# Optimization experiments

Measured on AMD Instinct MI355X. Metric: run time of the kernel, lower is better.

Reference implementation:

```python
import jax, jax.numpy as jnp
import numpy as np
from jax import lax

STEPS = 16
CHANNELS = 64
HIDDEN = 1024
LENGTH = 2048
BATCH = 32
EPS = 1e-5

def setup_inputs() -> dict:
    key = jax.random.key(0)
    ks = jax.random.split(key, 8)
    x = jax.random.normal(ks[0], (BATCH, CHANNELS, LENGTH), dtype=jnp.float32)
    # Conv1d params (PyTorch layout OIH for weights)
    s1 = 1.0 / np.sqrt(CHANNELS * 3)
    s2 = 1.0 / np.sqrt(HIDDEN)
    w1 = jax.random.uniform(ks[1], (HIDDEN, CHANNELS, 3), jnp.float32, -s1, s1)
    b1 = jax.random.uniform(ks[2], (HIDDEN,), jnp.float32, -s1, s1)
    w2 = jax.random.uniform(ks[3], (HIDDEN, HIDDEN), jnp.float32, -s2, s2)
    b2 = jax.random.uniform(ks[4], (HIDDEN,), jnp.float32, -s2, s2)
    w3 = jax.random.uniform(ks[5], (CHANNELS, HIDDEN), jnp.float32, -s2, s2)
    b3 = jax.random.uniform(ks[6], (CHANNELS,), jnp.float32, -s2, s2)
    # LayerNorm([channels, length]) elementwise affine
    gamma = jnp.ones((CHANNELS, LENGTH), dtype=jnp.float32)
    beta = jnp.zeros((CHANNELS, LENGTH), dtype=jnp.float32)
    return {"x": x, "w1": w1, "b1": b1, "w2": w2, "b2": b2,
            "w3": w3, "b3": b3, "gamma": gamma, "beta": beta}

def reference(x, w1, b1, w2, b2, w3, b3, gamma, beta):
    # Eval-mode forward: dropout is identity, no noise injection.
    def step(x, _):
        # conv1: k=3, pad=1  -> [B, HIDDEN, L]
        h = lax.conv_general_dilated(
            x, w1, window_strides=(1,), padding=[(1, 1)],
            dimension_numbers=("NCH", "OIH", "NCH"))
        h = jax.nn.relu(h + b1[None, :, None])
        # conv2: 1x1 (pointwise) -> GEMM over channel dim
        h = jnp.einsum("oh,bhl->bol", w2, h) + b2[None, :, None]
        h = jax.nn.relu(h)
        # conv3: 1x1 back to channels
        h = jnp.einsum("ch,bhl->bcl", w3, h) + b3[None, :, None]
        x = x + h  # residual
        # LayerNorm over [channels, length] per sample
        mu = jnp.mean(x, axis=(1, 2), keepdims=True)
        var = jnp.var(x, axis=(1, 2), keepdims=True)
        x = (x - mu) * lax.rsqrt(var + EPS) * gamma[None] + beta[None]
        return x, None

    x, _ = lax.scan(step, x, None, length=STEPS)
    return x
```

## Files before the change

### kernel.cpp

```cpp
#include <hip/hip_runtime.h>
#include <stdint.h>

#define L_LEN 2048
#define LP (L_LEN + 2)
#define CH 64
#define HID 1024
#define NSTEP 16
#define NB 32
#define EPS_F 1e-5f

typedef __bf16 bf16x8 __attribute__((ext_vector_type(8)));
typedef float f32x4 __attribute__((ext_vector_type(4)));

__device__ __forceinline__ float u16f(unsigned short u){
  unsigned int x = ((unsigned int)u) << 16;
  return __builtin_bit_cast(float, x);
}
__device__ __forceinline__ unsigned short f2u(float f){
  unsigned int x = __builtin_bit_cast(unsigned int, f);
  unsigned int r = x + 0x7FFFu + ((x >> 16) & 1u);
  return (unsigned short)(r >> 16);
}

__device__ __forceinline__ void gload16(const unsigned short* g, const unsigned short* l){
  __builtin_amdgcn_global_load_lds(
      (const __attribute__((address_space(1))) unsigned int*)g,
      (__attribute__((address_space(3))) unsigned int*)l, 16, 0, 0);
}

__global__ void flag_k(const unsigned int* __restrict__ gamma, int* __restrict__ flag){
  *flag = (gamma[0] == 0x3F803F80u) ? 1 : 0;
}

__global__ __launch_bounds__(256)
void conv_k(const void* __restrict__ src, unsigned short* __restrict__ dst, int n,
            const int* __restrict__ flagp){
  int fl = *flagp;
  for (int i = blockIdx.x * 256 + threadIdx.x; i < n; i += gridDim.x * 256){
    dst[i] = fl ? ((const unsigned short*)src)[i] : f2u(((const float*)src)[i]);
  }
}

__global__ __launch_bounds__(256)
void packw1_k(const void* __restrict__ w1, unsigned short* __restrict__ w1p,
              const int* __restrict__ flagp){
  int idx = blockIdx.x * 256 + threadIdx.x;
  int o = idx / 192;
  int r = idx - o * 192;
  int t = r >> 6;
  int c = r & 63;
  int sidx = (o * 64 + c) * 3 + t;
  w1p[idx] = (*flagp) ? ((const unsigned short*)w1)[sidx]
                      : f2u(((const float*)w1)[sidx]);
}

__global__ __launch_bounds__(256)
void pad_k(unsigned short* __restrict__ xbfT){
  int i = blockIdx.x * 256 + threadIdx.x;
  int s = i >> 7;
  int r = i & 127;
  size_t row = (r >> 6) ? (size_t)(LP - 1) : 0;
  xbfT[((size_t)s * LP + row) * CH + (r & 63)] = 0;
}

__global__ __launch_bounds__(256)
void init_k(const void* __restrict__ xin, float* __restrict__ xf,
            unsigned short* __restrict__ xbfT, const int* __restrict__ flagp){
  int t = blockIdx.x * 256 + threadIdx.x;
  size_t i0 = (size_t)t * 4;
  float4 f;
  if (*flagp){
    ushort4 v = *reinterpret_cast<const ushort4*>(&((const unsigned short*)xin)[i0]);
    f = make_float4(u16f(v.x), u16f(v.y), u16f(v.z), u16f(v.w));
  } else {
    f = *reinterpret_cast<const float4*>(&((const float*)xin)[i0]);
  }
  *reinterpret_cast<float4*>(&xf[i0]) = f;
  int s = (int)(i0 >> 17);
  int r = (int)(i0 & 131071);
  int c = r >> 11;
  int l = r & 2047;
  unsigned short* d = &xbfT[((size_t)s * LP + l + 1) * CH + c];
  d[0]      = f2u(f.x);
  d[CH]     = f2u(f.y);
  d[2 * CH] = f2u(f.z);
  d[3 * CH] = f2u(f.w);
}


template<int QM>
__device__ __forceinline__ void ld_a(const unsigned short* lb, int wm, int lane,
                                     bf16x8 (&af)[4][2]){
  #pragma unroll
  for (int i = 0; i < 4; i++)
    #pragma unroll
    for (int kk = 0; kk < 2; kk++){
      int r  = wm * 128 + QM * 64 + i * 16 + (lane & 15);
      int cb = kk * 4 + (lane >> 4);
      af[i][kk] = *reinterpret_cast<const bf16x8*>(lb + r * 64 + ((cb ^ (r & 7)) << 3));
    }
}
template<int QN>
__device__ __forceinline__ void ld_b(const unsigned short* lb, int wn, int lane,
                                     bf16x8 (&bfr)[2][2][2]){
  #pragma unroll
  for (int j = 0; j < 2; j++)
    #pragma unroll
    for (int kk = 0; kk < 2; kk++){
      int r  = wn * 64 + QN * 32 + j * 16 + (lane & 15);
      int cb = kk * 4 + (lane >> 4);
      bfr[QN][j][kk] = *reinterpret_cast<const bf16x8*>(lb + 16384 + r * 64 + ((cb ^ (r & 7)) << 3));
    }
}
template<int QM, int QN>
__device__ __forceinline__ void mfma_q(f32x4 (&acc)[8][4], bf16x8 (&af)[4][2],
                                       bf16x8 (&bfr)[2][2][2]){
  #pragma unroll
  for (int i = 0; i < 4; i++)
    #pragma unroll
    for (int j = 0; j < 2; j++)
      #pragma unroll
      for (int kk = 0; kk < 2; kk++)
        acc[QM * 4 + i][QN * 2 + j] = __builtin_amdgcn_mfma_f32_16x16x32_bf16(
            af[i][kk], bfr[QN][j][kk], acc[QM * 4 + i][QN * 2 + j], 0, 0, 0);
}

#define SYNC_MID() do { __builtin_amdgcn_s_barrier(); \
  asm volatile("s_waitcnt lgkmcnt(0)" ::: "memory"); \
  __builtin_amdgcn_sched_barrier(0); \
  __builtin_amdgcn_s_setprio(1); } while(0)
#define SYNC_END0() do { __builtin_amdgcn_s_setprio(0); \
  __builtin_amdgcn_s_barrier(); } while(0)
#define SYNC_ENDV() do { __builtin_amdgcn_s_setprio(0); \
  asm volatile("s_waitcnt vmcnt(4)" ::: "memory"); \
  __builtin_amdgcn_s_barrier(); } while(0)

__global__ __launch_bounds__(512, 2)
void gemm8_k(const unsigned short* __restrict__ A,
             const unsigned short* __restrict__ Bx,
             const unsigned short* __restrict__ bias,
             unsigned short* __restrict__ OutB)
{
  __shared__ __align__(16) unsigned short lds[65536];
  const int tid  = threadIdx.x;
  const int lane = tid & 63;
  const int wave = tid >> 6;
  const int wm   = wave >> 2;
  const int wn   = wave & 3;

  const int nwg = gridDim.x;
  const int bid = blockIdx.x;
  const int qq = nwg >> 3, rr = nwg & 7;
  const int xcd = bid & 7, loc = bid >> 3;
  const int wg = (xcd < rr) ? (xcd * (qq + 1) + loc)
                            : (rr * (qq + 1) + (xcd - rr) * qq + loc);
  const int bx = wg & 3;
  const int t_ = wg >> 2;
  const int by = t_ & 7;
  const int bb = t_ >> 3;
  const int m0 = bx * 256;
  const int n0 = by * 256;

  const unsigned short* Bb = Bx + (size_t)bb * L_LEN * HID;

  f32x4 acc[8][4];
  #pragma unroll
  for (int i = 0; i < 8; i++)
    #pragma unroll
    for (int j = 0; j < 4; j++)
      #pragma unroll
      for (int v = 0; v < 4; v++) acc[i][j][v] = 0.f;

  bf16x8 af[4][2];
  bf16x8 bfr[2][2][2];

  auto STAGE_A = [&](int t, int buf, int half){
    #pragma unroll
    for (int li = 0; li < 2; li++){
      int q = li * 512 + tid;
      int row = q >> 3, cc = q & 7;
      int scc = cc ^ (row & 7);
      gload16(&A[(size_t)(m0 + half * 128 + row) * HID + t * 64 + scc * 8],
              lds + buf * 32768 + half * 8192 + (li * 512 + wave * 64) * 8);
    }
  };
  auto STAGE_B = [&](int t, int buf, int half){
    #pragma unroll
    for (int li = 0; li < 2; li++){
      int q = li * 512 + tid;
      int row = q >> 3, cc = q & 7;
      int scc = cc ^ (row & 7);
      gload16(&Bb[(size_t)(n0 + half * 128 + row) * HID + t * 64 + scc * 8],
              lds + buf * 32768 + 16384 + half * 8192 + (li * 512 + wave * 64) * 8);
    }
  };

  const unsigned short* L0 = lds;
  const unsigned short* L1 = lds + 32768;

  STAGE_B(0, 0, 0); STAGE_B(0, 0, 1);
  STAGE_A(0, 0, 0); STAGE_A(0, 0, 1);
  STAGE_B(1, 1, 0); STAGE_B(1, 1, 1);
  asm volatile("s_waitcnt vmcnt(4)" ::: "memory");
  __builtin_amdgcn_s_barrier();

  for (int it = 0; it < 8; it++){
    int t1 = 2 * it + 1;
    int t2 = (2 * it + 2 < 16) ? 2 * it + 2 : 15;
    int t3 = (2 * it + 3 < 16) ? 2 * it + 3 : 15;
    ld_a<0>(L0, wm, lane, af); ld_b<0>(L0, wn, lane, bfr);
    STAGE_A(t1, 1, 0);
    SYNC_MID(); mfma_q<0, 0>(acc, af, bfr); SYNC_END0();
    ld_b<1>(L0, wn, lane, bfr);
    STAGE_A(t1, 1, 1);
    SYNC_MID(); mfma_q<0, 1>(acc, af, bfr); SYNC_END0();
    ld_a<1>(L0, wm, lane, af);
    STAGE_B(t2, 0, 0);
    SYNC_MID(); mfma_q<1, 0>(acc, af, bfr); SYNC_END0();
    STAGE_B(t2, 0, 1);
    SYNC_MID(); mfma_q<1, 1>(acc, af, bfr); SYNC_ENDV();
    ld_a<0>(L1, wm, lane, af); ld_b<0>(L1, wn, lane, bfr);
    STAGE_A(t2, 0, 0);
    SYNC_MID(); mfma_q<0, 0>(acc, af, bfr); SYNC_END0();
    ld_b<1>(L1, wn, lane, bfr);
    STAGE_A(t2, 0, 1);
    SYNC_MID(); mfma_q<0, 1>(acc, af, bfr); SYNC_END0();
    ld_a<1>(L1, wm, lane, af);
    STAGE_B(t3, 1, 0);
    SYNC_MID(); mfma_q<1, 0>(acc, af, bfr); SYNC_END0();
    STAGE_B(t3, 1, 1);
    SYNC_MID(); mfma_q<1, 1>(acc, af, bfr); SYNC_ENDV();
  }

  #pragma unroll
  for (int i = 0; i < 8; i++){
    int mb_ = m0 + wm * 128 + i * 16 + ((lane >> 4) << 2);
    float bv0 = u16f(bias[mb_ + 0]), bv1 = u16f(bias[mb_ + 1]);
    float bv2 = u16f(bias[mb_ + 2]), bv3 = u16f(bias[mb_ + 3]);
    #pragma unroll
    for (int j = 0; j < 4; j++){
      int n = n0 + wn * 64 + j * 16 + (lane & 15);
      ushort4 pk;
      pk.x = f2u(fmaxf(acc[i][j][0] + bv0, 0.f));
      pk.y = f2u(fmaxf(acc[i][j][1] + bv1, 0.f));
      pk.z = f2u(fmaxf(acc[i][j][2] + bv2, 0.f));
      pk.w = f2u(fmaxf(acc[i][j][3] + bv3, 0.f));
      *reinterpret_cast<ushort4*>(&OutB[((size_t)bb * L_LEN + n) * HID + mb_]) = pk;
    }
  }
}

template<int MODE, int BM, int BN, int WM_, int WN_>
__global__ __launch_bounds__(256)
void gemm_k(const unsigned short* __restrict__ A,
            const unsigned short* __restrict__ Bx,
            const unsigned short* __restrict__ bias,
            unsigned short* __restrict__ OutB,
            float* __restrict__ OutX,
            int K, int gx, int gy)
{
  constexpr int BK = 64;
  constexpr int FM = BM / (WM_ * 16);
  constexpr int FN = BN / (WN_ * 16);
  constexpr int ACH = (BM * 8) / 256;
  constexpr int BCH = (BN * 8) / 256;
  __shared__ __align__(16) unsigned short lA[BM * BK];
  __shared__ __align__(16) unsigned short lB[BN * BK];

  const int tid  = threadIdx.x;
  const int lane = tid & 63;
  const int wave = tid >> 6;
  const int wm = wave / WN_;
  const int wn = wave % WN_;

  const int nwg = gridDim.x;
  const int bid = blockIdx.x;
  const int qq = nwg >> 3, rr = nwg & 7;
  const int xcd = bid & 7, loc = bid >> 3;
  const int wg = (xcd < rr) ? (xcd * (qq + 1) + loc)
                            : (rr * (qq + 1) + (xcd - rr) * qq + loc);
  const int bx = wg % gx;
  const int t1 = wg / gx;
  const int by = t1 % gy;
  const int b  = t1 / gy;

  const int m0 = bx * BM;
  const int n0 = by * BN;

  f32x4 acc[FM][FN];
  #pragma unroll
  for (int i = 0; i < FM; i++)
    #pragma unroll
    for (int j = 0; j < FN; j++)
      #pragma unroll
      for (int v = 0; v < 4; v++) acc[i][j][v] = 0.f;

  for (int k0 = 0; k0 < K; k0 += BK){
    #pragma unroll
    for (int i = 0; i < ACH; i++){
      int q = tid + i * 256;
      int row = q >> 3;
      int cc  = q & 7;
      int scc = cc ^ (row & 7);
      gload16(&A[(size_t)(m0 + row) * K + k0 + scc * 8],
              &lA[(size_t)(i * 256 + wave * 64) * 8]);
    }
    #pragma unroll
    for (int i = 0; i < BCH; i++){
      int q = tid + i * 256;
      int row = q >> 3;
      int cc  = q & 7;
      int scc = cc ^ (row & 7);
      const unsigned short* gp;
      if (MODE == 0){
        gp = &Bx[((size_t)b * LP + n0 + row + (k0 >> 6)) * CH + scc * 8];
      } else {
        gp = &Bx[((size_t)b * L_LEN + n0 + row) * HID + k0 + scc * 8];
      }
      gload16(gp, &lB[(size_t)(i * 256 + wave * 64) * 8]);
    }
    __syncthreads();
    #pragma unroll
    for (int kk = 0; kk < BK / 32; kk++){
      bf16x8 af[FM], bfv[FN];
      int cbase = kk * 4 + (lane >> 4);
      #pragma unroll
      for (int i = 0; i < FM; i++){
        int row = wm * FM * 16 + i * 16 + (lane & 15);
        af[i] = *reinterpret_cast<const bf16x8*>(&lA[row * BK + ((cbase ^ (row & 7)) << 3)]);
      }
      #pragma unroll
      for (int j = 0; j < FN; j++){
        int row = wn * FN * 16 + j * 16 + (lane & 15);
        bfv[j] = *reinterpret_cast<const bf16x8*>(&lB[row * BK + ((cbase ^ (row & 7)) << 3)]);
      }
      #pragma unroll
      for (int i = 0; i < FM; i++)
        #pragma unroll
        for (int j = 0; j < FN; j++)
          acc[i][j] = __builtin_amdgcn_mfma_f32_16x16x32_bf16(af[i], bfv[j], acc[i][j], 0, 0, 0);
    }
    __syncthreads();
  }

  if (MODE <= 1){
    #pragma unroll
    for (int i = 0; i < FM; i++){
      int mb_ = m0 + wm * FM * 16 + i * 16 + ((lane >> 4) << 2);
      float bv0 = u16f(bias[mb_ + 0]), bv1 = u16f(bias[mb_ + 1]);
      float bv2 = u16f(bias[mb_ + 2]), bv3 = u16f(bias[mb_ + 3]);
      #pragma unroll
      for (int j = 0; j < FN; j++){
        int n = n0 + wn * FN * 16 + j * 16 + (lane & 15);
        ushort4 pk;
        pk.x = f2u(fmaxf(acc[i][j][0] + bv0, 0.f));
        pk.y = f2u(fmaxf(acc[i][j][1] + bv1, 0.f));
        pk.z = f2u(fmaxf(acc[i][j][2] + bv2, 0.f));
        pk.w = f2u(fmaxf(acc[i][j][3] + bv3, 0.f));
        *reinterpret_cast<ushort4*>(&OutB[((size_t)b * L_LEN + n) * HID + mb_]) = pk;
      }
    }
  } else {
    #pragma unroll
    for (int i = 0; i < FM; i++){
      int mb_ = m0 + wm * FM * 16 + i * 16 + ((lane >> 4) << 2);
      float bv[4] = { u16f(bias[mb_ + 0]), u16f(bias[mb_ + 1]),
                      u16f(bias[mb_ + 2]), u16f(bias[mb_ + 3]) };
      #pragma unroll
      for (int j = 0; j < FN; j++){
        int n = n0 + wn * FN * 16 + j * 16 + (lane & 15);
        #pragma unroll
        for (int v = 0; v < 4; v++){
          float* p = &OutX[((size_t)b * CH + mb_ + v) * L_LEN + n];
          *p = *p + acc[i][j][v] + bv[v];
        }
      }
    }
  }
}

__global__ __launch_bounds__(256)
void stats_k(const float* __restrict__ x, float2* __restrict__ part){
  int s = blockIdx.x, blk = blockIdx.y;
  const float4* base = reinterpret_cast<const float4*>(x + (size_t)s * (CH * L_LEN) + (size_t)blk * 8192);
  float sum = 0.f, sq = 0.f;
  #pragma unroll
  for (int i = 0; i < 8; i++){
    float4 v = base[threadIdx.x + i * 256];
    sum += v.x + v.y + v.z + v.w;
    sq  += v.x * v.x + v.y * v.y + v.z * v.z + v.w * v.w;
  }
  #pragma unroll
  for (int off = 32; off > 0; off >>= 1){
    sum += __shfl_xor(sum, off);
    sq  += __shfl_xor(sq, off);
  }
  __shared__ float2 wsum[4];
  if ((threadIdx.x & 63) == 0) wsum[threadIdx.x >> 6] = make_float2(sum, sq);
  __syncthreads();
  if (threadIdx.x == 0){
    float s0 = 0.f, s1 = 0.f;
    #pragma unroll
    for (int i = 0; i < 4; i++){ s0 += wsum[i].x; s1 += wsum[i].y; }
    part[s * 16 + blk] = make_float2(s0, s1);
  }
}

__global__ __launch_bounds__(256)
void ln_k(float* __restrict__ x, const float2* __restrict__ part,
          const unsigned short* __restrict__ gamma, const unsigned short* __restrict__ beta,
          unsigned short* __restrict__ xbfT, void* __restrict__ dout,
          const int* __restrict__ flagp, int last)
{
  int s = blockIdx.x;
  float sum = 0.f, sq = 0.f;
  #pragma unroll
  for (int i = 0; i < 16; i++){ float2 p = part[s * 16 + i]; sum += p.x; sq += p.y; }
  const float inv = 1.f / (float)(CH * L_LEN);
  float mean = sum * inv;
  float var  = fmaxf(sq * inv - mean * mean, 0.f);
  float rstd = rsqrtf(var + EPS_F);

  int i0 = (blockIdx.y * 256 + threadIdx.x) * 4;
  size_t g = (size_t)s * (CH * L_LEN) + i0;
  float4 v = *reinterpret_cast<const float4*>(&x[g]);
  ushort4 gm = *reinterpret_cast<const ushort4*>(&gamma[i0]);
  ushort4 bt = *reinterpret_cast<const ushort4*>(&beta[i0]);
  float o0 = (v.x - mean) * rstd * u16f(gm.x) + u16f(bt.x);
  float o1 = (v.y - mean) * rstd * u16f(gm.y) + u16f(bt.y);
  float o2 = (v.z - mean) * rstd * u16f(gm.z) + u16f(bt.z);
  float o3 = (v.w - mean) * rstd * u16f(gm.w) + u16f(bt.w);
  *reinterpret_cast<float4*>(&x[g]) = make_float4(o0, o1, o2, o3);
  if (last){
    if (*flagp){
      ushort4 pk = { f2u(o0), f2u(o1), f2u(o2), f2u(o3) };
      *reinterpret_cast<ushort4*>(&((unsigned short*)dout)[g]) = pk;
    } else {
      *reinterpret_cast<float4*>(&((float*)dout)[g]) = make_float4(o0, o1, o2, o3);
    }
  } else {
    int c = i0 >> 11;
    int l = i0 & 2047;
    unsigned short* d = &xbfT[((size_t)s * LP + l + 1) * CH + c];
    d[0]      = f2u(o0);
    d[CH]     = f2u(o1);
    d[2 * CH] = f2u(o2);
    d[3 * CH] = f2u(o3);
  }
}

extern "C" void kernel_launch(void* const* d_in, const int* in_sizes, int n_in,
                              void* d_out, int out_size, void* d_ws, size_t ws_size,
                              hipStream_t stream)
{
  const void* xin   = d_in[0];
  const void* w1    = d_in[1];
  const void* b1    = d_in[2];
  const void* w2    = d_in[3];
  const void* b2    = d_in[4];
  const void* w3    = d_in[5];
  const void* b3    = d_in[6];
  const void* gamma = d_in[7];
  const void* beta  = d_in[8];

  char* ws = (char*)d_ws;
  size_t off = 0;
  auto alloc = [&](size_t bytes)->char*{
    char* p = ws + off;
    off = (off + bytes + 255) & ~(size_t)255;
    return p;
  };

  float*          x_f32 = (float*)alloc((size_t)NB * CH * L_LEN * 4);
  unsigned short* xbfT  = (unsigned short*)alloc((size_t)NB * LP * CH * 2);
  unsigned short* w1p   = (unsigned short*)alloc((size_t)HID * 192 * 2);
  unsigned short* w2c   = (unsigned short*)alloc((size_t)HID * HID * 2);
  unsigned short* w3c   = (unsigned short*)alloc((size_t)CH * HID * 2);
  unsigned short* b1c   = (unsigned short*)alloc(HID * 2);
  unsigned short* b2c   = (unsigned short*)alloc(HID * 2);
  unsigned short* b3c   = (unsigned short*)alloc(CH * 2);
  unsigned short* gmc   = (unsigned short*)alloc((size_t)CH * L_LEN * 2);
  unsigned short* btc   = (unsigned short*)alloc((size_t)CH * L_LEN * 2);
  float2*         part  = (float2*)alloc(NB * 16 * sizeof(float2));
  int*            flag  = (int*)alloc(256);

  size_t rem = (ws_size > off) ? ws_size - off : 0;
  size_t per_b = (size_t)L_LEN * HID * 2 * 2;
  int bc = NB;
  while (bc > 1 && (size_t)bc * per_b > rem) bc >>= 1;
  unsigned short* h1 = (unsigned short*)(ws + off);
  unsigned short* h2 = h1 + (size_t)bc * L_LEN * HID;

  flag_k<<<1, 1, 0, stream>>>((const unsigned int*)gamma, flag);
  conv_k<<<4096, 256, 0, stream>>>(w2, w2c, HID * HID, flag);
  conv_k<<<256, 256, 0, stream>>>(w3, w3c, CH * HID, flag);
  conv_k<<<4, 256, 0, stream>>>(b1, b1c, HID, flag);
  conv_k<<<4, 256, 0, stream>>>(b2, b2c, HID, flag);
  conv_k<<<1, 256, 0, stream>>>(b3, b3c, CH, flag);
  conv_k<<<512, 256, 0, stream>>>(gamma, gmc, CH * L_LEN, flag);
  conv_k<<<512, 256, 0, stream>>>(beta, btc, CH * L_LEN, flag);
  packw1_k<<<768, 256, 0, stream>>>(w1, w1p, flag);
  pad_k<<<16, 256, 0, stream>>>(xbfT);
  init_k<<<4096, 256, 0, stream>>>(xin, x_f32, xbfT, flag);

  for (int step = 0; step < NSTEP; ++step){
    for (int cb = 0; cb < NB; cb += bc){
      gemm_k<0, 128, 128, 2, 2><<<dim3(8 * 16 * bc), 256, 0, stream>>>(
          w1p, xbfT + (size_t)cb * LP * CH, b1c, h1, nullptr, 192, 8, 16);
      gemm8_k<<<dim3(4 * 8 * bc), 512, 0, stream>>>(w2c, h1, b2c, h2);
      gemm_k<2, 64, 128, 1, 4><<<dim3(16 * bc), 256, 0, stream>>>(
          w3c, h2, b3c, nullptr, x_f32 + (size_t)cb * CH * L_LEN, HID, 1, 16);
    }
    stats_k<<<dim3(NB, 16), 256, 0, stream>>>(x_f32, part);
    ln_k<<<dim3(NB, 128), 256, 0, stream>>>(x_f32, part, gmc, btc, xbfT, d_out, flag,
                                            step == NSTEP - 1 ? 1 : 0);
  }
}
```

Before: 4.482 ms.

## Specialize conv1/conv3 GEMMs, reuse shifted conv window, fuse LN stats into conv3

Replaces the generic templated GEMM with two specialized kernels. The conv1 kernel loads the whole K=192 weight slab and a single 264-row activation window into LDS once, then reads shifted rows for the three taps instead of reloading B per tap, using 256x256 tiles with 512 threads. The conv3 kernel double-buffers its LDS tiles to overlap loads with MFMA and computes per-block sum and sum-of-squares in its residual epilogue, which removes the separate stats kernel and its re-read of x. The trade-offs are much larger LDS use in conv1, which lowers occupancy, and a larger restructuring of the tile and block mapping.

```diff
diff --git a/kernel.cpp b/kernel.cpp
--- a/kernel.cpp
+++ b/kernel.cpp
@@ -86,7 +86,6 @@
   d[2 * CH] = f2u(f.z);
   d[3 * CH] = f2u(f.w);
 }
-
 
 template<int QM>
 __device__ __forceinline__ void ld_a(const unsigned short* lb, int wm, int lane,
@@ -250,28 +249,19 @@
   }
 }
 
-template<int MODE, int BM, int BN, int WM_, int WN_>
-__global__ __launch_bounds__(256)
-void gemm_k(const unsigned short* __restrict__ A,
-            const unsigned short* __restrict__ Bx,
-            const unsigned short* __restrict__ bias,
-            unsigned short* __restrict__ OutB,
-            float* __restrict__ OutX,
-            int K, int gx, int gy)
+__global__ __launch_bounds__(512)
+void c1_k(const unsigned short* __restrict__ A,
+          const unsigned short* __restrict__ Bx,
+          const unsigned short* __restrict__ bias,
+          unsigned short* __restrict__ OutB)
 {
-  constexpr int BK = 64;
-  constexpr int FM = BM / (WM_ * 16);
-  constexpr int FN = BN / (WN_ * 16);
-  constexpr int ACH = (BM * 8) / 256;
-  constexpr int BCH = (BN * 8) / 256;
-  __shared__ __align__(16) unsigned short lA[BM * BK];
-  __shared__ __align__(16) unsigned short lB[BN * BK];
-
+  __shared__ __align__(16) unsigned short lA1[256 * 192];
+  __shared__ __align__(16) unsigned short lB1[264 * 64];
   const int tid  = threadIdx.x;
   const int lane = tid & 63;
   const int wave = tid >> 6;
-  const int wm = wave / WN_;
-  const int wn = wave % WN_;
+  const int wm   = wave >> 2;
+  const int wn   = wave & 3;
 
   const int nwg = gridDim.x;
   const int bid = blockIdx.x;
@@ -279,130 +269,198 @@
   const int xcd = bid & 7, loc = bid >> 3;
   const int wg = (xcd < rr) ? (xcd * (qq + 1) + loc)
                             : (rr * (qq + 1) + (xcd - rr) * qq + loc);
-  const int bx = wg % gx;
-  const int t1 = wg / gx;
-  const int by = t1 % gy;
-  const int b  = t1 / gy;
-
-  const int m0 = bx * BM;
-  const int n0 = by * BN;
-
-  f32x4 acc[FM][FN];
-  #pragma unroll
-  for (int i = 0; i < FM; i++)
-    #pragma unroll
-    for (int j = 0; j < FN; j++)
+  const int bx = wg & 3;
+  const int t_ = wg >> 2;
+  const int by = t_ & 7;
+  const int bb = t_ >> 3;
+  const int m0 = bx * 256;
+  const int n0 = by * 256;
+
+  #pragma unroll
+  for (int p = 0; p < 12; p++){
+    int q = p * 512 + tid;
+    int row = q / 24, cc = q % 24;
+    int scc = cc ^ (row & 7);
+    gload16(&A[(size_t)(m0 + row) * 192 + scc * 8], &lA1[(p * 512 + wave * 64) * 8]);
+  }
+  #pragma unroll
+  for (int p = 0; p < 4; p++){
+    int q = p * 512 + tid;
+    int row = q >> 3, cc = q & 7;
+    int scc = cc ^ (row & 7);
+    int srow = n0 + row; if (srow > LP - 1) srow = LP - 1;
+    gload16(&Bx[((size_t)bb * LP + srow) * CH + scc * 8], &lB1[(p * 512 + wave * 64) * 8]);
+  }
+  if (wave == 0){
+    int q = 2048 + lane;
+    int row = q >> 3, cc = q & 7;
+    int scc = cc ^ (row & 7);
+    int srow = n0 + row; if (srow > LP - 1) srow = LP - 1;
+    gload16(&Bx[((size_t)bb * LP + srow) * CH + scc * 8], &lB1[2048 * 8]);
+  }
+  asm volatile("s_waitcnt vmcnt(0)" ::: "memory");
+  __builtin_amdgcn_s_barrier();
+
+  f32x4 acc[8][4];
+  #pragma unroll
+  for (int i = 0; i < 8; i++)
+    #pragma unroll
+    for (int j = 0; j < 4; j++)
       #pragma unroll
       for (int v = 0; v < 4; v++) acc[i][j][v] = 0.f;
 
-  for (int k0 = 0; k0 < K; k0 += BK){
-    #pragma unroll
-    for (int i = 0; i < ACH; i++){
-      int q = tid + i * 256;
-      int row = q >> 3;
-      int cc  = q & 7;
+  #pragma unroll
+  for (int t = 0; t < 3; t++){
+    #pragma unroll
+    for (int kk = 0; kk < 2; kk++){
+      bf16x8 af[8], bf[4];
+      int cb  = t * 8 + kk * 4 + (lane >> 4);
+      int cb2 = kk * 4 + (lane >> 4);
+      #pragma unroll
+      for (int i = 0; i < 8; i++){
+        int r = wm * 128 + i * 16 + (lane & 15);
+        af[i] = *reinterpret_cast<const bf16x8*>(&lA1[r * 192 + ((cb ^ (r & 7)) << 3)]);
+      }
+      #pragma unroll
+      for (int j = 0; j < 4; j++){
+        int r = wn * 64 + j * 16 + (lane & 15) + t;
+        bf[j] = *reinterpret_cast<const bf16x8*>(&lB1[r * 64 + ((cb2 ^ (r & 7)) << 3)]);
+      }
+      #pragma unroll
+      for (int i = 0; i < 8; i++)
+        #pragma unroll
+        for (int j = 0; j < 4; j++)
+          acc[i][j] = __builtin_amdgcn_mfma_f32_16x16x32_bf16(af[i], bf[j], acc[i][j], 0, 0, 0);
+    }
+  }
+
+  #pragma unroll
+  for (int i = 0; i < 8; i++){
+    int mb_ = m0 + wm * 128 + i * 16 + ((lane >> 4) << 2);
+    float bv0 = u16f(bias[mb_ + 0]), bv1 = u16f(bias[mb_ + 1]);
+    float bv2 = u16f(bias[mb_ + 2]), bv3 = u16f(bias[mb_ + 3]);
+    #pragma unroll
+    for (int j = 0; j < 4; j++){
+      int n = n0 + wn * 64 + j * 16 + (lane & 15);
+      ushort4 pk;
+      pk.x = f2u(fmaxf(acc[i][j][0] + bv0, 0.f));
+      pk.y = f2u(fmaxf(acc[i][j][1] + bv1, 0.f));
+      pk.z = f2u(fmaxf(acc[i][j][2] + bv2, 0.f));
+      pk.w = f2u(fmaxf(acc[i][j][3] + bv3, 0.f));
+      *reinterpret_cast<ushort4*>(&OutB[((size_t)bb * L_LEN + n) * HID + mb_]) = pk;
+    }
+  }
+}
+
+__global__ __launch_bounds__(256)
+void c3_k(const unsigned short* __restrict__ A,
+          const unsigned short* __restrict__ Bx,
+          const unsigned short* __restrict__ bias,
+          float* __restrict__ OutX,
+          float2* __restrict__ part)
+{
+  __shared__ __align__(16) unsigned short lA2[2][64 * 64];
+  __shared__ __align__(16) unsigned short lB2[2][128 * 64];
+  __shared__ float2 wsum[4];
+  const int tid  = threadIdx.x;
+  const int lane = tid & 63;
+  const int wave = tid >> 6;
+  const int wn   = wave;
+
+  const int nwg = gridDim.x;
+  const int bid = blockIdx.x;
+  const int qq = nwg >> 3, rr = nwg & 7;
+  const int xcd = bid & 7, loc = bid >> 3;
+  const int wg = (xcd < rr) ? (xcd * (qq + 1) + loc)
+                            : (rr * (qq + 1) + (xcd - rr) * qq + loc);
+  const int by = wg & 15;
+  const int bb = wg >> 4;
+  const int n0 = by * 128;
+
+  auto STAGE = [&](int t, int buf){
+    #pragma unroll
+    for (int i = 0; i < 2; i++){
+      int q = i * 256 + tid;
+      int row = q >> 3, cc = q & 7;
       int scc = cc ^ (row & 7);
-      gload16(&A[(size_t)(m0 + row) * K + k0 + scc * 8],
-              &lA[(size_t)(i * 256 + wave * 64) * 8]);
-    }
-    #pragma unroll
-    for (int i = 0; i < BCH; i++){
-      int q = tid + i * 256;
-      int row = q >> 3;
-      int cc  = q & 7;
+      gload16(&A[(size_t)row * HID + t * 64 + scc * 8], &lA2[buf][(i * 256 + wave * 64) * 8]);
+    }
+    #pragma unroll
+    for (int i = 0; i < 4; i++){
+      int q = i * 256 + tid;
+      int row = q >> 3, cc = q & 7;
       int scc = cc ^ (row & 7);
-      const unsigned short* gp;
-      if (MODE == 0){
-        gp = &Bx[((size_t)b * LP + n0 + row + (k0 >> 6)) * CH + scc * 8];
-      } else {
-        gp = &Bx[((size_t)b * L_LEN + n0 + row) * HID + k0 + scc * 8];
+      gload16(&Bx[((size_t)bb * L_LEN + n0 + row) * HID + t * 64 + scc * 8],
+              &lB2[buf][(i * 256 + wave * 64) * 8]);
+    }
+  };
+
+  f32x4 acc[4][2];
+  #pragma unroll
+  for (int i = 0; i < 4; i++)
+    #pragma unroll
+    for (int j = 0; j < 2; j++)
+      #pragma unroll
+      for (int v = 0; v < 4; v++) acc[i][j][v] = 0.f;
+
+  STAGE(0, 0);
+  __syncthreads();
+  for (int t = 0; t < 16; t++){
+    int cur = t & 1;
+    if (t < 15) STAGE(t + 1, cur ^ 1);
+    #pragma unroll
+    for (int kk = 0; kk < 2; kk++){
+      bf16x8 af[4], bf[2];
+      int cb = kk * 4 + (lane >> 4);
+      #pragma unroll
+      for (int i = 0; i < 4; i++){
+        int r = i * 16 + (lane & 15);
+        af[i] = *reinterpret_cast<const bf16x8*>(&lA2[cur][r * 64 + ((cb ^ (r & 7)) << 3)]);
       }
-      gload16(gp, &lB[(size_t)(i * 256 + wave * 64) * 8]);
+      #pragma unroll
+      for (int j = 0; j < 2; j++){
+        int r = wn * 32 + j * 16 + (lane & 15);
+        bf[j] = *reinterpret_cast<const bf16x8*>(&lB2[cur][r * 64 + ((cb ^ (r & 7)) << 3)]);
+      }
+      #pragma unroll
+      for (int i = 0; i < 4; i++)
+        #pragma unroll
+        for (int j = 0; j < 2; j++)
+          acc[i][j] = __builtin_amdgcn_mfma_f32_16x16x32_bf16(af[i], bf[j], acc[i][j], 0, 0, 0);
     }
     __syncthreads();
-    #pragma unroll
-    for (int kk = 0; kk < BK / 32; kk++){
-      bf16x8 af[FM], bfv[FN];
-      int cbase = kk * 4 + (lane >> 4);
-      #pragma unroll
-      for (int i = 0; i < FM; i++){
-        int row = wm * FM * 16 + i * 16 + (lane & 15);
-        af[i] = *reinterpret_cast<const bf16x8*>(&lA[row * BK + ((cbase ^ (row & 7)) << 3)]);
+  }
+
+  float lsum = 0.f, lsq = 0.f;
+  #pragma unroll
+  for (int i = 0; i < 4; i++){
+    int c0 = i * 16 + ((lane >> 4) << 2);
+    float bv[4] = { u16f(bias[c0 + 0]), u16f(bias[c0 + 1]),
+                    u16f(bias[c0 + 2]), u16f(bias[c0 + 3]) };
+    #pragma unroll
+    for (int j = 0; j < 2; j++){
+      int n = n0 + wn * 32 + j * 16 + (lane & 15);
+      #pragma unroll
+      for (int v = 0; v < 4; v++){
+        float* p = &OutX[((size_t)bb * CH + c0 + v) * L_LEN + n];
+        float val = *p + acc[i][j][v] + bv[v];
+        *p = val;
+        lsum += val; lsq += val * val;
       }
-      #pragma unroll
-      for (int j = 0; j < FN; j++){
-        int row = wn * FN * 16 + j * 16 + (lane & 15);
-        bfv[j] = *reinterpret_cast<const bf16x8*>(&lB[row * BK + ((cbase ^ (row & 7)) << 3)]);
-      }
-      #pragma unroll
-      for (int i = 0; i < FM; i++)
-        #pragma unroll
-        for (int j = 0; j < FN; j++)
-          acc[i][j] = __builtin_amdgcn_mfma_f32_16x16x32_bf16(af[i], bfv[j], acc[i][j], 0, 0, 0);
-    }
-    __syncthreads();
-  }
-
-  if (MODE <= 1){
-    #pragma unroll
-    for (int i = 0; i < FM; i++){
-      int mb_ = m0 + wm * FM * 16 + i * 16 + ((lane >> 4) << 2);
-      float bv0 = u16f(bias[mb_ + 0]), bv1 = u16f(bias[mb_ + 1]);
-      float bv2 = u16f(bias[mb_ + 2]), bv3 = u16f(bias[mb_ + 3]);
-      #pragma unroll
-      for (int j = 0; j < FN; j++){
-        int n = n0 + wn * FN * 16 + j * 16 + (lane & 15);
-        ushort4 pk;
-        pk.x = f2u(fmaxf(acc[i][j][0] + bv0, 0.f));
-        pk.y = f2u(fmaxf(acc[i][j][1] + bv1, 0.f));
-        pk.z = f2u(fmaxf(acc[i][j][2] + bv2, 0.f));
-        pk.w = f2u(fmaxf(acc[i][j][3] + bv3, 0.f));
-        *reinterpret_cast<ushort4*>(&OutB[((size_t)b * L_LEN + n) * HID + mb_]) = pk;
-      }
-    }
-  } else {
-    #pragma unroll
-    for (int i = 0; i < FM; i++){
-      int mb_ = m0 + wm * FM * 16 + i * 16 + ((lane >> 4) << 2);
-      float bv[4] = { u16f(bias[mb_ + 0]), u16f(bias[mb_ + 1]),
-                      u16f(bias[mb_ + 2]), u16f(bias[mb_ + 3]) };
-      #pragma unroll
-      for (int j = 0; j < FN; j++){
-        int n = n0 + wn * FN * 16 + j * 16 + (lane & 15);
-        #pragma unroll
-        for (int v = 0; v < 4; v++){
-          float* p = &OutX[((size_t)b * CH + mb_ + v) * L_LEN + n];
-          *p = *p + acc[i][j][v] + bv[v];
-        }
-      }
-    }
-  }
-}
-
-__global__ __launch_bounds__(256)
-void stats_k(const float* __restrict__ x, float2* __restrict__ part){
-  int s = blockIdx.x, blk = blockIdx.y;
-  const float4* base = reinterpret_cast<const float4*>(x + (size_t)s * (CH * L_LEN) + (size_t)blk * 8192);
-  float sum = 0.f, sq = 0.f;
-  #pragma unroll
-  for (int i = 0; i < 8; i++){
-    float4 v = base[threadIdx.x + i * 256];
-    sum += v.x + v.y + v.z + v.w;
-    sq  += v.x * v.x + v.y * v.y + v.z * v.z + v.w * v.w;
+    }
   }
   #pragma unroll
   for (int off = 32; off > 0; off >>= 1){
-    sum += __shfl_xor(sum, off);
-    sq  += __shfl_xor(sq, off);
-  }
-  __shared__ float2 wsum[4];
-  if ((threadIdx.x & 63) == 0) wsum[threadIdx.x >> 6] = make_float2(sum, sq);
+    lsum += __shfl_xor(lsum, off);
+    lsq  += __shfl_xor(lsq, off);
+  }
+  if (lane == 0) wsum[wave] = make_float2(lsum, lsq);
   __syncthreads();
-  if (threadIdx.x == 0){
+  if (tid == 0){
     float s0 = 0.f, s1 = 0.f;
     #pragma unroll
     for (int i = 0; i < 4; i++){ s0 += wsum[i].x; s1 += wsum[i].y; }
-    part[s * 16 + blk] = make_float2(s0, s1);
+    part[bb * 16 + by] = make_float2(s0, s1);
   }
 }
 
@@ -505,13 +563,12 @@
 
   for (int step = 0; step < NSTEP; ++step){
     for (int cb = 0; cb < NB; cb += bc){
-      gemm_k<0, 128, 128, 2, 2><<<dim3(8 * 16 * bc), 256, 0, stream>>>(
-          w1p, xbfT + (size_t)cb * LP * CH, b1c, h1, nullptr, 192, 8, 16);
+      c1_k<<<dim3(4 * 8 * bc), 512, 0, stream>>>(
+          w1p, xbfT + (size_t)cb * LP * CH, b1c, h1);
       gemm8_k<<<dim3(4 * 8 * bc), 512, 0, stream>>>(w2c, h1, b2c, h2);
-      gemm_k<2, 64, 128, 1, 4><<<dim3(16 * bc), 256, 0, stream>>>(
-          w3c, h2, b3c, nullptr, x_f32 + (size_t)cb * CH * L_LEN, HID, 1, 16);
-    }
-    stats_k<<<dim3(NB, 16), 256, 0, stream>>>(x_f32, part);
+      c3_k<<<dim3(16 * bc), 256, 0, stream>>>(
+          w3c, h2, b3c, x_f32 + (size_t)cb * CH * L_LEN, part + (size_t)cb * 16);
+    }
     ln_k<<<dim3(NB, 128), 256, 0, stream>>>(x_f32, part, gmc, btc, xbfT, d_out, flag,
                                             step == NSTEP - 1 ? 1 : 0);
   }
```

New measurement: 4.191 ms. 6.5% less time.
